# Optimization experiments

Measured on AMD Instinct MI355X. Metric: run time of the kernel, lower is better.

Reference implementation:

```python
import jax, jax.numpy as jnp
import numpy as np

N_TX, N_CARD, N_MERCH = 200000, 50000, 10000
E = 200000
TX_IN, EMB, H = 128, 64, 128
N_LAYERS, N_ETYPES = 2, 4  # etypes: 0 card->tx, 1 tx->card, 2 merch->tx, 3 tx->merch


def setup_inputs() -> dict:
    key = jax.random.key(0)
    ks = jax.random.split(key, 24)
    s = 0.05
    inp = {
        "tx_x": jax.random.normal(ks[0], (N_TX, TX_IN), jnp.float32),
        "card_ids": jnp.arange(N_CARD, dtype=jnp.int64),
        "merch_ids": jnp.arange(N_MERCH, dtype=jnp.int64),
        "e_card": jax.random.randint(ks[1], (E,), 0, N_CARD),
        "e_tx_c": jnp.arange(E, dtype=jnp.int64),
        "e_merch": jax.random.randint(ks[2], (E,), 0, N_MERCH),
        "e_tx_m": jnp.arange(E, dtype=jnp.int64),
        # parameters
        "card_emb": jax.random.normal(ks[3], (N_CARD, EMB), jnp.float32) * s,
        "merch_emb": jax.random.normal(ks[4], (N_MERCH, EMB), jnp.float32) * s,
        "card_proj_W": jax.random.normal(ks[5], (EMB, H), jnp.float32) * s,
        "card_proj_b": jnp.zeros((H,), jnp.float32),
        "merch_proj_W": jax.random.normal(ks[6], (EMB, H), jnp.float32) * s,
        "merch_proj_b": jnp.zeros((H,), jnp.float32),
        "tx_W": jax.random.normal(ks[7], (TX_IN, H), jnp.float32) * s,
        "tx_b": jnp.zeros((H,), jnp.float32),
        "conv_Wl": jax.random.normal(ks[8], (N_LAYERS, N_ETYPES, H, H), jnp.float32) * s,
        "conv_bl": jnp.zeros((N_LAYERS, N_ETYPES, H), jnp.float32),
        "conv_Wr": jax.random.normal(ks[9], (N_LAYERS, N_ETYPES, H, H), jnp.float32) * s,
        "h1_W": jax.random.normal(ks[10], (H, H), jnp.float32) * s,
        "h1_b": jnp.zeros((H,), jnp.float32),
        "h2_W": jax.random.normal(ks[11], (H, 1), jnp.float32) * s,
        "h2_b": jnp.zeros((1,), jnp.float32),
    }
    return inp


def _sage(x_src, x_dst, src, dst, Wl, bl, Wr, n_dst):
    # PyG SAGEConv: mean-aggregate neighbor features, then lin_l(agg)+lin_r(x_dst)
    agg = jax.ops.segment_sum(x_src[src], dst, num_segments=n_dst)
    cnt = jax.ops.segment_sum(jnp.ones((src.shape[0],), x_src.dtype), dst, num_segments=n_dst)
    mean = agg / jnp.maximum(cnt, 1.0)[:, None]
    return mean @ Wl + bl + x_dst @ Wr


def reference(tx_x, card_ids, merch_ids, e_card, e_tx_c, e_merch, e_tx_m,
              card_emb, merch_emb, card_proj_W, card_proj_b, merch_proj_W, merch_proj_b,
              tx_W, tx_b, conv_Wl, conv_bl, conv_Wr, h1_W, h1_b, h2_W, h2_b):
    # input encoders (dropout inactive at eval)
    h_tx = jax.nn.relu(tx_x @ tx_W + tx_b)
    h_card = card_emb[card_ids] @ card_proj_W + card_proj_b
    h_merch = merch_emb[merch_ids] @ merch_proj_W + merch_proj_b

    for l in range(N_LAYERS):
        Wl, bl, Wr = conv_Wl[l], conv_bl[l], conv_Wr[l]
        # HeteroConv aggr='sum' across edge types sharing a dst type
        o_tx = (_sage(h_card, h_tx, e_card, e_tx_c, Wl[0], bl[0], Wr[0], N_TX)
                + _sage(h_merch, h_tx, e_merch, e_tx_m, Wl[2], bl[2], Wr[2], N_TX))
        o_card = _sage(h_tx, h_card, e_tx_c, e_card, Wl[1], bl[1], Wr[1], N_CARD)
        o_merch = _sage(h_tx, h_merch, e_tx_m, e_merch, Wl[3], bl[3], Wr[3], N_MERCH)
        h_tx, h_card, h_merch = jax.nn.relu(o_tx), jax.nn.relu(o_card), jax.nn.relu(o_merch)

    logits = (jax.nn.relu(h_tx @ h1_W + h1_b) @ h2_W + h2_b).reshape(-1)
    return logits
```

## Files before the change

### kernel.cpp

```cpp
#include <hip/hip_runtime.h>


#define N_TX    200000
#define N_CARD  50000
#define N_MERCH 10000
#define NE      200000

typedef __attribute__((ext_vector_type(8))) short short8;
typedef __attribute__((ext_vector_type(4))) float f32x4;

__device__ inline unsigned short f2b(float f) {
    unsigned u = __builtin_bit_cast(unsigned, f);
    unsigned r = (u + 0x7fffu + ((u >> 16) & 1u)) >> 16;
    return (unsigned short)r;
}
__device__ inline float b2f(unsigned short s) {
    return __builtin_bit_cast(float, (unsigned)s << 16);
}

__global__ __launch_bounds__(256, 3) void fused2(
    const void* __restrict__ A, int a_f32,
    const unsigned short* __restrict__ W1T, const float* __restrict__ b1,
    const unsigned short* __restrict__ W2T, const float* __restrict__ b2,
    const unsigned short* __restrict__ P1, const int* __restrict__ I1,
    const unsigned short* __restrict__ P2, const int* __restrict__ I2,
    unsigned short* __restrict__ OUT0,
    const float* __restrict__ h2w, const float* __restrict__ h2b,
    void* __restrict__ OUT1, int M)
{
    __shared__ float Tf[64 * 132];
    __shared__ unsigned short Tb[64 * 136];
    const int tid  = threadIdx.x;
    const int wave = tid >> 6;
    const int lane = tid & 63;
    const int quad = lane >> 4;
    const int l15  = lane & 15;
    const int base = blockIdx.x * 64;
    const int rgrp = tid >> 4;
    const int c0   = l15 * 8;
    const bool modeA = (OUT0 != nullptr);

    int idx1[4], idx2[4];
#pragma unroll
    for (int p = 0; p < 4; ++p) {
        int r = base + p * 16 + rgrp;
        int rc = (r < M) ? r : 0;
        idx1[p] = I1 ? I1[rc] : 0;
        idx2[p] = I2 ? I2[rc] : 0;
    }

    short8 af[4];
    {
        int r = base + wave * 16 + l15;
        int rc = (r < M) ? r : 0;
        if (a_f32) {
            const float* ap = (const float*)A + (size_t)rc * 128 + quad * 8;
#pragma unroll
            for (int kk = 0; kk < 4; ++kk) {
                float4 u = *reinterpret_cast<const float4*>(ap + kk * 32);
                float4 v = *reinterpret_cast<const float4*>(ap + kk * 32 + 4);
                short8 t;
                t[0] = (short)f2b(u.x); t[1] = (short)f2b(u.y);
                t[2] = (short)f2b(u.z); t[3] = (short)f2b(u.w);
                t[4] = (short)f2b(v.x); t[5] = (short)f2b(v.y);
                t[6] = (short)f2b(v.z); t[7] = (short)f2b(v.w);
                af[kk] = t;
            }
        } else {
            const unsigned short* ap =
                (const unsigned short*)A + (size_t)rc * 128 + quad * 8;
#pragma unroll
            for (int kk = 0; kk < 4; ++kk)
                af[kk] = *reinterpret_cast<const short8*>(ap + kk * 32);
        }
    }

    f32x4 acc[8];
#pragma unroll
    for (int nt = 0; nt < 8; ++nt) acc[nt] = (f32x4){0.f, 0.f, 0.f, 0.f};
#pragma unroll
    for (int nt = 0; nt < 8; ++nt) {
        const unsigned short* bp = W1T + (nt * 16 + l15) * 128 + quad * 8;
#pragma unroll
        for (int kk = 0; kk < 4; ++kk) {
            short8 bf = *reinterpret_cast<const short8*>(bp + kk * 32);
            acc[nt] = __builtin_amdgcn_mfma_f32_16x16x32_bf16(
                af[kk], bf, acc[nt], 0, 0, 0);
        }
    }

    short8 p1v[4], p2v[4];
    if (P1) {
#pragma unroll
        for (int p = 0; p < 4; ++p)
            p1v[p] = *reinterpret_cast<const short8*>(
                P1 + (size_t)idx1[p] * 128 + c0);
    }
    if (P2) {
#pragma unroll
        for (int p = 0; p < 4; ++p)
            p2v[p] = *reinterpret_cast<const short8*>(
                P2 + (size_t)idx2[p] * 128 + c0);
    }

    const int lrow0 = wave * 16 + quad * 4;
    if (modeA) {
#pragma unroll
        for (int nt = 0; nt < 8; ++nt) {
            float bb = b1 ? b1[nt * 16 + l15] : 0.f;
#pragma unroll
            for (int reg = 0; reg < 4; ++reg)
                Tb[(lrow0 + reg) * 136 + nt * 16 + l15] =
                    f2b(fmaxf(acc[nt][reg] + bb, 0.f));
        }
    } else {
#pragma unroll
        for (int nt = 0; nt < 8; ++nt)
#pragma unroll
            for (int reg = 0; reg < 4; ++reg)
                Tf[(lrow0 + reg) * 132 + nt * 16 + l15] = acc[nt][reg];
    }
    __syncthreads();

    if (modeA) {
#pragma unroll
        for (int p = 0; p < 4; ++p) {
            const int rloc = p * 16 + rgrp;
            const int r = base + rloc;
            if (r < M) {
                short8 hv = *reinterpret_cast<const short8*>(&Tb[rloc * 136 + c0]);
                *reinterpret_cast<short8*>(OUT0 + (size_t)r * 128 + c0) = hv;
            }
        }
    } else {
        float b1r[8];
#pragma unroll
        for (int j = 0; j < 8; ++j) b1r[j] = b1 ? b1[c0 + j] : 0.f;
#pragma unroll
        for (int p = 0; p < 4; ++p) {
            const int rloc = p * 16 + rgrp;
            float4 u = *reinterpret_cast<const float4*>(&Tf[rloc * 132 + c0]);
            float4 v = *reinterpret_cast<const float4*>(&Tf[rloc * 132 + c0 + 4]);
            float o[8] = {u.x, u.y, u.z, u.w, v.x, v.y, v.z, v.w};
            short8 ov;
#pragma unroll
            for (int j = 0; j < 8; ++j) {
                float t = o[j] + b1r[j];
                if (P1) t += b2f((unsigned short)p1v[p][j]);
                if (P2) t += b2f((unsigned short)p2v[p][j]);
                ov[j] = (short)f2b(fmaxf(t, 0.f));
            }
            *reinterpret_cast<short8*>(&Tb[rloc * 136 + c0]) = ov;
        }
        __syncthreads();
    }

    short8 af2[4];
#pragma unroll
    for (int kk = 0; kk < 4; ++kk)
        af2[kk] = *reinterpret_cast<const short8*>(
            &Tb[(wave * 16 + l15) * 136 + quad * 8 + kk * 32]);

    f32x4 acc2[8];
#pragma unroll
    for (int nt = 0; nt < 8; ++nt) acc2[nt] = (f32x4){0.f, 0.f, 0.f, 0.f};
#pragma unroll
    for (int nt = 0; nt < 8; ++nt) {
        const unsigned short* bp = W2T + (nt * 16 + l15) * 128 + quad * 8;
#pragma unroll
        for (int kk = 0; kk < 4; ++kk) {
            short8 bf = *reinterpret_cast<const short8*>(bp + kk * 32);
            acc2[nt] = __builtin_amdgcn_mfma_f32_16x16x32_bf16(
                af2[kk], bf, acc2[nt], 0, 0, 0);
        }
    }

    if (!modeA) {
        float hsum[4] = {0.f, 0.f, 0.f, 0.f};
#pragma unroll
        for (int nt = 0; nt < 8; ++nt) {
            float bb = b2 ? b2[nt * 16 + l15] : 0.f;
            float w = h2w[nt * 16 + l15];
#pragma unroll
            for (int reg = 0; reg < 4; ++reg) {
                float o = fmaxf(acc2[nt][reg] + bb, 0.f);
                hsum[reg] += o * w;
            }
        }
        float* OUTf = (float*)OUT1;
#pragma unroll
        for (int reg = 0; reg < 4; ++reg) {
            float h = hsum[reg];
            h += __shfl_xor(h, 1);
            h += __shfl_xor(h, 2);
            h += __shfl_xor(h, 4);
            h += __shfl_xor(h, 8);
            int r = base + wave * 16 + quad * 4 + reg;
            if (l15 == 0 && r < M) OUTf[r] = h + h2b[0];
        }
    } else {
#pragma unroll
        for (int nt = 0; nt < 8; ++nt)
#pragma unroll
            for (int reg = 0; reg < 4; ++reg)
                Tf[(lrow0 + reg) * 132 + nt * 16 + l15] = acc2[nt][reg];
        __syncthreads();
        float b2r[8];
#pragma unroll
        for (int j = 0; j < 8; ++j) b2r[j] = b2 ? b2[c0 + j] : 0.f;
        unsigned short* OB = (unsigned short*)OUT1;
#pragma unroll
        for (int p = 0; p < 4; ++p) {
            const int rloc = p * 16 + rgrp;
            const int r = base + rloc;
            float4 u = *reinterpret_cast<const float4*>(&Tf[rloc * 132 + c0]);
            float4 v = *reinterpret_cast<const float4*>(&Tf[rloc * 132 + c0 + 4]);
            float o[8] = {u.x, u.y, u.z, u.w, v.x, v.y, v.z, v.w};
            short8 ov;
#pragma unroll
            for (int j = 0; j < 8; ++j) {
                float t = o[j] + b2r[j];
                if (P1) t += b2f((unsigned short)p1v[p][j]);
                if (P2) t += b2f((unsigned short)p2v[p][j]);
                ov[j] = (short)f2b(fmaxf(t, 0.f));
            }
            if (r < M)
                *reinterpret_cast<short8*>(OB + (size_t)r * 128 + c0) = ov;
        }
    }
}

__global__ __launch_bounds__(256, 3) void fusedE(
    const float* __restrict__ A, int K1,
    const unsigned short* __restrict__ W1T, const float* __restrict__ b1,
    const unsigned short* __restrict__ W2T,
    unsigned short* __restrict__ OUT0, unsigned short* __restrict__ OUT1, int M)
{
    __shared__ float Tf[64 * 132];
    __shared__ unsigned short Tb[64 * 136];
    const int tid  = threadIdx.x;
    const int wave = tid >> 6;
    const int lane = tid & 63;
    const int quad = lane >> 4;
    const int l15  = lane & 15;
    const int base = blockIdx.x * 64;
    const int rgrp = tid >> 4;
    const int c0   = l15 * 8;
    const int nkk  = K1 >> 5;

    short8 af[4];
    {
        int r = base + wave * 16 + l15;
        int rc = (r < M) ? r : 0;
        const float* ap = A + (size_t)rc * K1 + quad * 8;
#pragma unroll
        for (int kk = 0; kk < 4; ++kk) if (kk < nkk) {
            float4 u = *reinterpret_cast<const float4*>(ap + kk * 32);
            float4 v = *reinterpret_cast<const float4*>(ap + kk * 32 + 4);
            short8 t;
            t[0] = (short)f2b(u.x); t[1] = (short)f2b(u.y);
            t[2] = (short)f2b(u.z); t[3] = (short)f2b(u.w);
            t[4] = (short)f2b(v.x); t[5] = (short)f2b(v.y);
            t[6] = (short)f2b(v.z); t[7] = (short)f2b(v.w);
            af[kk] = t;
        }
    }

    f32x4 acc[8];
#pragma unroll
    for (int nt = 0; nt < 8; ++nt) acc[nt] = (f32x4){0.f, 0.f, 0.f, 0.f};
#pragma unroll
    for (int nt = 0; nt < 8; ++nt) {
        const unsigned short* bp = W1T + (nt * 16 + l15) * K1 + quad * 8;
#pragma unroll
        for (int kk = 0; kk < 4; ++kk) if (kk < nkk) {
            short8 bf = *reinterpret_cast<const short8*>(bp + kk * 32);
            acc[nt] = __builtin_amdgcn_mfma_f32_16x16x32_bf16(
                af[kk], bf, acc[nt], 0, 0, 0);
        }
    }

    const int lrow0 = wave * 16 + quad * 4;
#pragma unroll
    for (int nt = 0; nt < 8; ++nt) {
        float bb = b1 ? b1[nt * 16 + l15] : 0.f;
#pragma unroll
        for (int reg = 0; reg < 4; ++reg)
            Tb[(lrow0 + reg) * 136 + nt * 16 + l15] = f2b(acc[nt][reg] + bb);
    }
    __syncthreads();

#pragma unroll
    for (int p = 0; p < 4; ++p) {
        const int rloc = p * 16 + rgrp;
        const int r = base + rloc;
        if (r < M) {
            short8 hv = *reinterpret_cast<const short8*>(&Tb[rloc * 136 + c0]);
            *reinterpret_cast<short8*>(OUT0 + (size_t)r * 128 + c0) = hv;
        }
    }

    short8 af2[4];
#pragma unroll
    for (int kk = 0; kk < 4; ++kk)
        af2[kk] = *reinterpret_cast<const short8*>(
            &Tb[(wave * 16 + l15) * 136 + quad * 8 + kk * 32]);

    f32x4 acc2[8];
#pragma unroll
    for (int nt = 0; nt < 8; ++nt) acc2[nt] = (f32x4){0.f, 0.f, 0.f, 0.f};
#pragma unroll
    for (int nt = 0; nt < 8; ++nt) {
        const unsigned short* bp = W2T + (nt * 16 + l15) * 128 + quad * 8;
#pragma unroll
        for (int kk = 0; kk < 4; ++kk) {
            short8 bf = *reinterpret_cast<const short8*>(bp + kk * 32);
            acc2[nt] = __builtin_amdgcn_mfma_f32_16x16x32_bf16(
                af2[kk], bf, acc2[nt], 0, 0, 0);
        }
    }
#pragma unroll
    for (int nt = 0; nt < 8; ++nt)
#pragma unroll
        for (int reg = 0; reg < 4; ++reg)
            Tf[(lrow0 + reg) * 132 + nt * 16 + l15] = acc2[nt][reg];
    __syncthreads();
#pragma unroll
    for (int p = 0; p < 4; ++p) {
        const int rloc = p * 16 + rgrp;
        const int r = base + rloc;
        if (r >= M) continue;
        float4 u = *reinterpret_cast<const float4*>(&Tf[rloc * 132 + c0]);
        float4 v = *reinterpret_cast<const float4*>(&Tf[rloc * 132 + c0 + 4]);
        float o[8] = {u.x, u.y, u.z, u.w, v.x, v.y, v.z, v.w};
        short8 ov;
#pragma unroll
        for (int j = 0; j < 8; ++j) ov[j] = (short)f2b(o[j]);
        *reinterpret_cast<short8*>(OUT1 + (size_t)r * 128 + c0) = ov;
    }
}

__global__ __launch_bounds__(256, 3) void fusedU(
    const unsigned short* __restrict__ A1, const unsigned short* __restrict__ A2,
    const unsigned short* __restrict__ W1aT, const unsigned short* __restrict__ W1bT,
    const float* __restrict__ b1,
    const unsigned short* __restrict__ W2T,
    unsigned short* __restrict__ OUT1, int M)
{
    __shared__ float Tf[64 * 132];
    __shared__ unsigned short Tb[64 * 136];
    const int tid  = threadIdx.x;
    const int wave = tid >> 6;
    const int lane = tid & 63;
    const int quad = lane >> 4;
    const int l15  = lane & 15;
    const int base = blockIdx.x * 64;
    const int rgrp = tid >> 4;
    const int c0   = l15 * 8;

    short8 afa[4], afb[4];
    {
        int r = base + wave * 16 + l15;
        int rc = (r < M) ? r : 0;
        const unsigned short* a1 = A1 + (size_t)rc * 128 + quad * 8;
        const unsigned short* a2 = A2 + (size_t)rc * 128 + quad * 8;
#pragma unroll
        for (int kk = 0; kk < 4; ++kk) {
            afa[kk] = *reinterpret_cast<const short8*>(a1 + kk * 32);
            afb[kk] = *reinterpret_cast<const short8*>(a2 + kk * 32);
        }
    }

    f32x4 acc[8];
#pragma unroll
    for (int nt = 0; nt < 8; ++nt) acc[nt] = (f32x4){0.f, 0.f, 0.f, 0.f};
#pragma unroll
    for (int nt = 0; nt < 8; ++nt) {
        const unsigned short* bpa = W1aT + (nt * 16 + l15) * 128 + quad * 8;
        const unsigned short* bpb = W1bT + (nt * 16 + l15) * 128 + quad * 8;
#pragma unroll
        for (int kk = 0; kk < 4; ++kk) {
            short8 ba = *reinterpret_cast<const short8*>(bpa + kk * 32);
            acc[nt] = __builtin_amdgcn_mfma_f32_16x16x32_bf16(
                afa[kk], ba, acc[nt], 0, 0, 0);
            short8 bb = *reinterpret_cast<const short8*>(bpb + kk * 32);
            acc[nt] = __builtin_amdgcn_mfma_f32_16x16x32_bf16(
                afb[kk], bb, acc[nt], 0, 0, 0);
        }
    }

    const int lrow0 = wave * 16 + quad * 4;
#pragma unroll
    for (int nt = 0; nt < 8; ++nt) {
        float bv = b1 ? b1[nt * 16 + l15] : 0.f;
#pragma unroll
        for (int reg = 0; reg < 4; ++reg)
            Tb[(lrow0 + reg) * 136 + nt * 16 + l15] =
                f2b(fmaxf(acc[nt][reg] + bv, 0.f));
    }
    __syncthreads();

    short8 af2[4];
#pragma unroll
    for (int kk = 0; kk < 4; ++kk)
        af2[kk] = *reinterpret_cast<const short8*>(
            &Tb[(wave * 16 + l15) * 136 + quad * 8 + kk * 32]);

    f32x4 acc2[8];
#pragma unroll
    for (int nt = 0; nt < 8; ++nt) acc2[nt] = (f32x4){0.f, 0.f, 0.f, 0.f};
#pragma unroll
    for (int nt = 0; nt < 8; ++nt) {
        const unsigned short* bp = W2T + (nt * 16 + l15) * 128 + quad * 8;
#pragma unroll
        for (int kk = 0; kk < 4; ++kk) {
            short8 bf = *reinterpret_cast<const short8*>(bp + kk * 32);
            acc2[nt] = __builtin_amdgcn_mfma_f32_16x16x32_bf16(
                af2[kk], bf, acc2[nt], 0, 0, 0);
        }
    }
#pragma unroll
    for (int nt = 0; nt < 8; ++nt)
#pragma unroll
        for (int reg = 0; reg < 4; ++reg)
            Tf[(lrow0 + reg) * 132 + nt * 16 + l15] = acc2[nt][reg];
    __syncthreads();
#pragma unroll
    for (int p = 0; p < 4; ++p) {
        const int rloc = p * 16 + rgrp;
        const int r = base + rloc;
        if (r >= M) continue;
        float4 u = *reinterpret_cast<const float4*>(&Tf[rloc * 132 + c0]);
        float4 v = *reinterpret_cast<const float4*>(&Tf[rloc * 132 + c0 + 4]);
        float o[8] = {u.x, u.y, u.z, u.w, v.x, v.y, v.z, v.w};
        short8 ov;
#pragma unroll
        for (int j = 0; j < 8; ++j) ov[j] = (short)f2b(o[j]);
        *reinterpret_cast<short8*>(OUT1 + (size_t)r * 128 + c0) = ov;
    }
}

__global__ __launch_bounds__(256) void convert_weights(
    const float* __restrict__ tx_W, const float* __restrict__ card_proj_W,
    const float* __restrict__ merch_proj_W, const float* __restrict__ h1_W,
    const float* __restrict__ conv_Wl, const float* __restrict__ conv_Wr,
    const float* __restrict__ conv_bl,
    unsigned short* __restrict__ WT, float* __restrict__ bsum)
{
    int job = blockIdx.y;
    int K = 128;
    const float* src = nullptr;
    const float* src2 = nullptr;
    if (job == 0) src = tx_W;
    else if (job == 1) { src = card_proj_W; K = 64; }
    else if (job == 2) { src = merch_proj_W; K = 64; }
    else if (job == 3) src = h1_W;
    else {
        int l = (job - 4) / 7, e = (job - 4) % 7;
        const float* Wl = conv_Wl + (size_t)l * 4 * 16384;
        const float* Wr = conv_Wr + (size_t)l * 4 * 16384;
        switch (e) {
            case 0: src = Wl; break;
            case 1: src = Wl + 16384; break;
            case 2: src = Wl + 2 * 16384; break;
            case 3: src = Wl + 3 * 16384; break;
            case 4: src = Wr + 16384; break;
            case 5: src = Wr + 3 * 16384; break;
            default:
                src = Wr; src2 = Wr + 2 * 16384;
                if (blockIdx.x == 0 && threadIdx.x < 128) {
                    const float* bl = conv_bl + (size_t)l * 4 * 128;
                    bsum[l * 128 + threadIdx.x] =
                        bl[threadIdx.x] + bl[2 * 128 + threadIdx.x];
                }
                break;
        }
    }
    int e = blockIdx.x * 256 + threadIdx.x;
    if (e < (K << 7)) {
        int n = (K == 128) ? (e >> 7) : (e >> 6);
        int k = e & (K - 1);
        float v = src[(size_t)k * 128 + n];
        if (src2) v += src2[(size_t)k * 128 + n];
        WT[(size_t)job * 16384 + n * K + k] = f2b(v);
    }
}

__global__ __launch_bounds__(256) void hist_kernel(
    const int* __restrict__ e_card, const int* __restrict__ e_merch,
    int* __restrict__ hist_c, int* __restrict__ hist_m, int E)
{
    int i = blockIdx.x * 256 + threadIdx.x;
    if (i < E) {
        atomicAdd(&hist_c[e_card[i]], 1);
        atomicAdd(&hist_m[e_merch[i]], 1);
    }
}

__global__ __launch_bounds__(1024) void scan2_kernel(
    const int* __restrict__ hist_c, int* __restrict__ offs_c, int* __restrict__ cur_c, int nc,
    const int* __restrict__ hist_m, int* __restrict__ offs_m, int* __restrict__ cur_m, int nm)
{
    const int* hist = (blockIdx.x == 0) ? hist_c : hist_m;
    int* offs = (blockIdx.x == 0) ? offs_c : offs_m;
    int* cursor = (blockIdx.x == 0) ? cur_c : cur_m;
    int n = (blockIdx.x == 0) ? nc : nm;
    __shared__ int wsum[16];
    __shared__ int s_carry;
    const int tid = threadIdx.x, lane = tid & 63, wid = tid >> 6;
    if (tid == 0) s_carry = 0;
    __syncthreads();
    for (int base = 0; base < n; base += 1024) {
        int i = base + tid;
        int v = (i < n) ? hist[i] : 0;
        int x = v;
#pragma unroll
        for (int d = 1; d < 64; d <<= 1) {
            int t = __shfl_up(x, d);
            if (lane >= d) x += t;
        }
        if (lane == 63) wsum[wid] = x;
        __syncthreads();
        if (wid == 0) {
            int y = (lane < 16) ? wsum[lane] : 0;
#pragma unroll
            for (int d = 1; d < 16; d <<= 1) {
                int t = __shfl_up(y, d);
                if (lane >= d) y += t;
            }
            if (lane < 16) wsum[lane] = y;
        }
        __syncthreads();
        int wbase = (wid > 0) ? wsum[wid - 1] : 0;
        int excl = s_carry + wbase + x - v;
        if (i < n) { offs[i] = excl; cursor[i] = excl; }
        __syncthreads();
        if (tid == 0) s_carry += wsum[15];
        __syncthreads();
    }
    if (threadIdx.x == 0) offs[n] = s_carry;
}

__global__ __launch_bounds__(256) void place_kernel(
    const int* __restrict__ e_card, const int* __restrict__ e_tx_c,
    const int* __restrict__ e_merch, const int* __restrict__ e_tx_m,
    int* __restrict__ cur_c, int* __restrict__ eidx_c,
    int* __restrict__ cur_m, int* __restrict__ eidx_m, int E)
{
    int i = blockIdx.x * 256 + threadIdx.x;
    if (i < E) {
        int pc = atomicAdd(&cur_c[e_card[i]], 1);
        eidx_c[pc] = e_tx_c[i];
        int pm = atomicAdd(&cur_m[e_merch[i]], 1);
        eidx_m[pm] = e_tx_m[i];
    }
}

__global__ __launch_bounds__(256) void gather_mean(
    const unsigned short* __restrict__ h_src, const int* __restrict__ offs,
    const int* __restrict__ eidx, unsigned short* __restrict__ out_mean, int n_dst)
{
    const int lane = threadIdx.x & 63;
    const int l15 = lane & 15;
    const int quad = lane >> 4;
    const int d = blockIdx.x * 4 + (threadIdx.x >> 6);
    if (d >= n_dst) return;
    const int s = offs[d], e = offs[d + 1];
    float a[8] = {0.f, 0.f, 0.f, 0.f, 0.f, 0.f, 0.f, 0.f};
    for (int p = s + quad; p < e; p += 4) {
        int tx = eidx[p];
        short8 v = *reinterpret_cast<const short8*>(
            h_src + (size_t)tx * 128 + l15 * 8);
#pragma unroll
        for (int j = 0; j < 8; ++j) a[j] += b2f((unsigned short)v[j]);
    }
#pragma unroll
    for (int j = 0; j < 8; ++j) {
        a[j] += __shfl_xor(a[j], 16);
        a[j] += __shfl_xor(a[j], 32);
    }
    if (quad == 0) {
        const float inv = (e > s) ? 1.0f / (float)(e - s) : 0.f;
        short8 o;
#pragma unroll
        for (int j = 0; j < 8; ++j) o[j] = (short)f2b(a[j] * inv);
        *reinterpret_cast<short8*>(out_mean + (size_t)d * 128 + l15 * 8) = o;
    }
}

extern "C" void kernel_launch(void* const* d_in, const int* in_sizes, int n_in,
                              void* d_out, int out_size, void* d_ws, size_t ws_size,
                              hipStream_t stream)
{
    const float* tx_x        = (const float*)d_in[0];
    const int*   e_card      = (const int*)d_in[3];
    const int*   e_tx_c      = (const int*)d_in[4];
    const int*   e_merch     = (const int*)d_in[5];
    const int*   e_tx_m      = (const int*)d_in[6];
    const float* card_emb    = (const float*)d_in[7];
    const float* merch_emb   = (const float*)d_in[8];
    const float* card_proj_W = (const float*)d_in[9];
    const float* card_proj_b = (const float*)d_in[10];
    const float* merch_proj_W= (const float*)d_in[11];
    const float* merch_proj_b= (const float*)d_in[12];
    const float* tx_W        = (const float*)d_in[13];
    const float* tx_b        = (const float*)d_in[14];
    const float* conv_Wl     = (const float*)d_in[15];
    const float* conv_bl     = (const float*)d_in[16];
    const float* conv_Wr     = (const float*)d_in[17];
    const float* h1_W        = (const float*)d_in[18];
    const float* h1_b        = (const float*)d_in[19];
    const float* h2_W        = (const float*)d_in[20];
    const float* h2_b        = (const float*)d_in[21];

    char* wsb = (char*)d_ws;
    auto alloc = [&](size_t bytes) {
        char* p = wsb; wsb += (bytes + 255) & ~(size_t)255; return p;
    };
    unsigned short* h_tx0      = (unsigned short*)alloc((size_t)N_TX * 128 * 2);
    unsigned short* h_tx1      = (unsigned short*)alloc((size_t)N_TX * 128 * 2);
    unsigned short* h_card0    = (unsigned short*)alloc((size_t)N_CARD * 128 * 2);
    unsigned short* h_merch0   = (unsigned short*)alloc((size_t)N_MERCH * 128 * 2);
    unsigned short* p_card     = (unsigned short*)alloc((size_t)N_CARD * 128 * 2);
    unsigned short* p_merch    = (unsigned short*)alloc((size_t)N_MERCH * 128 * 2);
    unsigned short* mean_card  = (unsigned short*)alloc((size_t)N_CARD * 128 * 2);
    unsigned short* mean_merch = (unsigned short*)alloc((size_t)N_MERCH * 128 * 2);
    unsigned short* WT         = (unsigned short*)alloc((size_t)18 * 16384 * 2);
    float* bsum = (float*)alloc(2 * 128 * 4);
    int* hist_c = (int*)alloc((size_t)(N_CARD + N_MERCH) * 4);
    int* hist_m = hist_c + N_CARD;
    int* offs_c = (int*)alloc((size_t)(N_CARD + 1) * 4);
    int* cur_c  = (int*)alloc((size_t)N_CARD * 4);
    int* eidx_c = (int*)alloc((size_t)NE * 4);
    int* offs_m = (int*)alloc((size_t)(N_MERCH + 1) * 4);
    int* cur_m  = (int*)alloc((size_t)N_MERCH * 4);
    int* eidx_m = (int*)alloc((size_t)NE * 4);

    auto WTj = [&](int job) { return WT + (size_t)job * 16384; };

    convert_weights<<<dim3(64, 18), dim3(256), 0, stream>>>(
        tx_W, card_proj_W, merch_proj_W, h1_W, conv_Wl, conv_Wr, conv_bl,
        WT, bsum);
    hipMemsetAsync(hist_c, 0, (size_t)(N_CARD + N_MERCH) * 4, stream);
    hist_kernel<<<dim3((NE + 255) / 256), dim3(256), 0, stream>>>(
        e_card, e_merch, hist_c, hist_m, NE);
    scan2_kernel<<<dim3(2), dim3(1024), 0, stream>>>(
        hist_c, offs_c, cur_c, N_CARD, hist_m, offs_m, cur_m, N_MERCH);
    place_kernel<<<dim3((NE + 255) / 256), dim3(256), 0, stream>>>(
        e_card, e_tx_c, e_merch, e_tx_m, cur_c, eidx_c, cur_m, eidx_m, NE);

    fusedE<<<dim3((N_CARD + 63) / 64), dim3(256), 0, stream>>>(
        card_emb, 64, WTj(1), card_proj_b, WTj(4), h_card0, p_card, N_CARD);
    fusedE<<<dim3((N_MERCH + 63) / 64), dim3(256), 0, stream>>>(
        merch_emb, 64, WTj(2), merch_proj_b, WTj(6), h_merch0, p_merch, N_MERCH);

    fused2<<<dim3((N_TX + 63) / 64), dim3(256), 0, stream>>>(
        tx_x, 1, WTj(0), tx_b, WTj(10), bsum,
        p_card, e_card, p_merch, e_merch,
        h_tx0, nullptr, nullptr, h_tx1, N_TX);

    gather_mean<<<dim3((N_CARD + 3) / 4), dim3(256), 0, stream>>>(
        h_tx0, offs_c, eidx_c, mean_card, N_CARD);
    gather_mean<<<dim3((N_MERCH + 3) / 4), dim3(256), 0, stream>>>(
        h_tx0, offs_m, eidx_m, mean_merch, N_MERCH);

    fusedU<<<dim3((N_CARD + 63) / 64), dim3(256), 0, stream>>>(
        mean_card, h_card0, WTj(5), WTj(8), conv_bl + 128, WTj(11),
        p_card, N_CARD);
    fusedU<<<dim3((N_MERCH + 63) / 64), dim3(256), 0, stream>>>(
        mean_merch, h_merch0, WTj(7), WTj(9), conv_bl + 3 * 128, WTj(13),
        p_merch, N_MERCH);

    fused2<<<dim3((N_TX + 63) / 64), dim3(256), 0, stream>>>(
        h_tx1, 0, WTj(17), bsum + 128, WTj(3), h1_b,
        p_card, e_card, p_merch, e_merch,
        nullptr, h2_W, h2_b, d_out, N_TX);
}
```

Measured before the change: 675.6 us.

## Fuse gather-mean into update kernel, merge card/merchant launches, vectorize scan

Moves the neighbor mean aggregation into the per-node update GEMM kernel, so mean results stay in shared memory instead of round-tripping through global buffers. Card and merchant work are merged into single launches that pick their parameters by block index, and the embedding kernel is specialized to K=64. The prefix scan now has each thread handle 8 elements, cutting the number of block-wide iterations. The fused gather runs inside 64-row GEMM blocks, which may lower parallelism for the irregular gather and serializes 16 rows per wave.

Measured after the change: 713.9 us. +5.7%, slower.

```diff
diff --git a/kernel.cpp b/kernel.cpp
--- a/kernel.cpp
+++ b/kernel.cpp
@@ -230,31 +230,44 @@
     }
 }
 
-__global__ __launch_bounds__(256, 3) void fusedE(
-    const float* __restrict__ A, int K1,
-    const unsigned short* __restrict__ W1T, const float* __restrict__ b1,
-    const unsigned short* __restrict__ W2T,
-    unsigned short* __restrict__ OUT0, unsigned short* __restrict__ OUT1, int M)
+__global__ __launch_bounds__(256, 3) void fusedE_both(
+    const float* __restrict__ Ac, const unsigned short* __restrict__ W1Tc,
+    const float* __restrict__ b1c, const unsigned short* __restrict__ W2Tc,
+    unsigned short* __restrict__ OUT0c, unsigned short* __restrict__ OUT1c,
+    int Mc, int nbc,
+    const float* __restrict__ Am, const unsigned short* __restrict__ W1Tm,
+    const float* __restrict__ b1m, const unsigned short* __restrict__ W2Tm,
+    unsigned short* __restrict__ OUT0m, unsigned short* __restrict__ OUT1m,
+    int Mm)
 {
     __shared__ float Tf[64 * 132];
     __shared__ unsigned short Tb[64 * 136];
+    const bool isC = (int)blockIdx.x < nbc;
+    const int bx   = isC ? blockIdx.x : blockIdx.x - nbc;
+    const float* A = isC ? Ac : Am;
+    const unsigned short* W1T = isC ? W1Tc : W1Tm;
+    const float* b1 = isC ? b1c : b1m;
+    const unsigned short* W2T = isC ? W2Tc : W2Tm;
+    unsigned short* OUT0 = isC ? OUT0c : OUT0m;
+    unsigned short* OUT1 = isC ? OUT1c : OUT1m;
+    const int M = isC ? Mc : Mm;
+
     const int tid  = threadIdx.x;
     const int wave = tid >> 6;
     const int lane = tid & 63;
     const int quad = lane >> 4;
     const int l15  = lane & 15;
-    const int base = blockIdx.x * 64;
+    const int base = bx * 64;
     const int rgrp = tid >> 4;
     const int c0   = l15 * 8;
-    const int nkk  = K1 >> 5;
-
-    short8 af[4];
+
+    short8 af[2];
     {
         int r = base + wave * 16 + l15;
         int rc = (r < M) ? r : 0;
-        const float* ap = A + (size_t)rc * K1 + quad * 8;
-#pragma unroll
-        for (int kk = 0; kk < 4; ++kk) if (kk < nkk) {
+        const float* ap = A + (size_t)rc * 64 + quad * 8;
+#pragma unroll
+        for (int kk = 0; kk < 2; ++kk) {
             float4 u = *reinterpret_cast<const float4*>(ap + kk * 32);
             float4 v = *reinterpret_cast<const float4*>(ap + kk * 32 + 4);
             short8 t;
@@ -271,9 +284,9 @@
     for (int nt = 0; nt < 8; ++nt) acc[nt] = (f32x4){0.f, 0.f, 0.f, 0.f};
 #pragma unroll
     for (int nt = 0; nt < 8; ++nt) {
-        const unsigned short* bp = W1T + (nt * 16 + l15) * K1 + quad * 8;
-#pragma unroll
-        for (int kk = 0; kk < 4; ++kk) if (kk < nkk) {
+        const unsigned short* bp = W1T + (nt * 16 + l15) * 64 + quad * 8;
+#pragma unroll
+        for (int kk = 0; kk < 2; ++kk) {
             short8 bf = *reinterpret_cast<const short8*>(bp + kk * 32);
             acc[nt] = __builtin_amdgcn_mfma_f32_16x16x32_bf16(
                 af[kk], bf, acc[nt], 0, 0, 0);
@@ -340,33 +353,78 @@
     }
 }
 
-__global__ __launch_bounds__(256, 3) void fusedU(
-    const unsigned short* __restrict__ A1, const unsigned short* __restrict__ A2,
-    const unsigned short* __restrict__ W1aT, const unsigned short* __restrict__ W1bT,
-    const float* __restrict__ b1,
-    const unsigned short* __restrict__ W2T,
-    unsigned short* __restrict__ OUT1, int M)
+__global__ __launch_bounds__(256, 3) void fusedU2_both(
+    const unsigned short* __restrict__ h_src,
+    const int* __restrict__ offs_c, const int* __restrict__ eidx_c,
+    const unsigned short* __restrict__ A2c,
+    const unsigned short* __restrict__ W1aTc, const unsigned short* __restrict__ W1bTc,
+    const float* __restrict__ b1c, const unsigned short* __restrict__ W2Tc,
+    unsigned short* __restrict__ OUTc, int Mc, int nbc,
+    const int* __restrict__ offs_m, const int* __restrict__ eidx_m,
+    const unsigned short* __restrict__ A2m,
+    const unsigned short* __restrict__ W1aTm, const unsigned short* __restrict__ W1bTm,
+    const float* __restrict__ b1m, const unsigned short* __restrict__ W2Tm,
+    unsigned short* __restrict__ OUTm, int Mm)
 {
     __shared__ float Tf[64 * 132];
     __shared__ unsigned short Tb[64 * 136];
+    const bool isC = (int)blockIdx.x < nbc;
+    const int bx   = isC ? blockIdx.x : blockIdx.x - nbc;
+    const int* offs = isC ? offs_c : offs_m;
+    const int* eidx = isC ? eidx_c : eidx_m;
+    const unsigned short* A2 = isC ? A2c : A2m;
+    const unsigned short* W1aT = isC ? W1aTc : W1aTm;
+    const unsigned short* W1bT = isC ? W1bTc : W1bTm;
+    const float* b1 = isC ? b1c : b1m;
+    const unsigned short* W2T = isC ? W2Tc : W2Tm;
+    unsigned short* OUT1 = isC ? OUTc : OUTm;
+    const int M = isC ? Mc : Mm;
+
     const int tid  = threadIdx.x;
     const int wave = tid >> 6;
     const int lane = tid & 63;
     const int quad = lane >> 4;
     const int l15  = lane & 15;
-    const int base = blockIdx.x * 64;
+    const int base = bx * 64;
     const int rgrp = tid >> 4;
     const int c0   = l15 * 8;
+
+    for (int n = 0; n < 16; ++n) {
+        const int d = base + wave * 16 + n;
+        int s = 0, e = 0;
+        if (d < M) { s = offs[d]; e = offs[d + 1]; }
+        float a[8] = {0.f, 0.f, 0.f, 0.f, 0.f, 0.f, 0.f, 0.f};
+        for (int p = s + quad; p < e; p += 4) {
+            int tx = eidx[p];
+            short8 v = *reinterpret_cast<const short8*>(
+                h_src + (size_t)tx * 128 + l15 * 8);
+#pragma unroll
+            for (int j = 0; j < 8; ++j) a[j] += b2f((unsigned short)v[j]);
+        }
+#pragma unroll
+        for (int j = 0; j < 8; ++j) {
+            a[j] += __shfl_xor(a[j], 16);
+            a[j] += __shfl_xor(a[j], 32);
+        }
+        if (quad == 0 && d < M) {
+            const float inv = (e > s) ? 1.0f / (float)(e - s) : 0.f;
+            short8 o;
+#pragma unroll
+            for (int j = 0; j < 8; ++j) o[j] = (short)f2b(a[j] * inv);
+            *reinterpret_cast<short8*>(&Tb[(wave * 16 + n) * 136 + l15 * 8]) = o;
+        }
+    }
+    __syncthreads();
 
     short8 afa[4], afb[4];
     {
         int r = base + wave * 16 + l15;
         int rc = (r < M) ? r : 0;
-        const unsigned short* a1 = A1 + (size_t)rc * 128 + quad * 8;
         const unsigned short* a2 = A2 + (size_t)rc * 128 + quad * 8;
 #pragma unroll
         for (int kk = 0; kk < 4; ++kk) {
-            afa[kk] = *reinterpret_cast<const short8*>(a1 + kk * 32);
+            afa[kk] = *reinterpret_cast<const short8*>(
+                &Tb[(wave * 16 + l15) * 136 + quad * 8 + kk * 32]);
             afb[kk] = *reinterpret_cast<const short8*>(a2 + kk * 32);
         }
     }
@@ -388,6 +446,7 @@
                 afb[kk], bb, acc[nt], 0, 0, 0);
         }
     }
+    __syncthreads();
 
     const int lrow0 = wave * 16 + quad * 4;
 #pragma unroll
@@ -510,10 +569,17 @@
     const int tid = threadIdx.x, lane = tid & 63, wid = tid >> 6;
     if (tid == 0) s_carry = 0;
     __syncthreads();
-    for (int base = 0; base < n; base += 1024) {
-        int i = base + tid;
-        int v = (i < n) ? hist[i] : 0;
-        int x = v;
+    for (int base = 0; base < n; base += 8192) {
+        const int i0 = base + tid * 8;
+        int v[8];
+        int tot = 0;
+#pragma unroll
+        for (int j = 0; j < 8; ++j) {
+            int idx = i0 + j;
+            v[j] = (idx < n) ? hist[idx] : 0;
+            tot += v[j];
+        }
+        int x = tot;
 #pragma unroll
         for (int d = 1; d < 64; d <<= 1) {
             int t = __shfl_up(x, d);
@@ -532,8 +598,13 @@
         }
         __syncthreads();
         int wbase = (wid > 0) ? wsum[wid - 1] : 0;
-        int excl = s_carry + wbase + x - v;
-        if (i < n) { offs[i] = excl; cursor[i] = excl; }
+        int run = s_carry + wbase + x - tot;
+#pragma unroll
+        for (int j = 0; j < 8; ++j) {
+            int idx = i0 + j;
+            if (idx < n) { offs[idx] = run; cursor[idx] = run; }
+            run += v[j];
+        }
         __syncthreads();
         if (tid == 0) s_carry += wsum[15];
         __syncthreads();
@@ -553,38 +624,6 @@
         eidx_c[pc] = e_tx_c[i];
         int pm = atomicAdd(&cur_m[e_merch[i]], 1);
         eidx_m[pm] = e_tx_m[i];
-    }
-}
-
-__global__ __launch_bounds__(256) void gather_mean(
-    const unsigned short* __restrict__ h_src, const int* __restrict__ offs,
-    const int* __restrict__ eidx, unsigned short* __restrict__ out_mean, int n_dst)
-{
-    const int lane = threadIdx.x & 63;
-    const int l15 = lane & 15;
-    const int quad = lane >> 4;
-    const int d = blockIdx.x * 4 + (threadIdx.x >> 6);
-    if (d >= n_dst) return;
-    const int s = offs[d], e = offs[d + 1];
-    float a[8] = {0.f, 0.f, 0.f, 0.f, 0.f, 0.f, 0.f, 0.f};
-    for (int p = s + quad; p < e; p += 4) {
-        int tx = eidx[p];
-        short8 v = *reinterpret_cast<const short8*>(
-            h_src + (size_t)tx * 128 + l15 * 8);
-#pragma unroll
-        for (int j = 0; j < 8; ++j) a[j] += b2f((unsigned short)v[j]);
-    }
-#pragma unroll
-    for (int j = 0; j < 8; ++j) {
-        a[j] += __shfl_xor(a[j], 16);
-        a[j] += __shfl_xor(a[j], 32);
-    }
-    if (quad == 0) {
-        const float inv = (e > s) ? 1.0f / (float)(e - s) : 0.f;
-        short8 o;
-#pragma unroll
-        for (int j = 0; j < 8; ++j) o[j] = (short)f2b(a[j] * inv);
-        *reinterpret_cast<short8*>(out_mean + (size_t)d * 128 + l15 * 8) = o;
     }
 }
 
@@ -617,15 +656,13 @@
     auto alloc = [&](size_t bytes) {
         char* p = wsb; wsb += (bytes + 255) & ~(size_t)255; return p;
     };
-    unsigned short* h_tx0      = (unsigned short*)alloc((size_t)N_TX * 128 * 2);
-    unsigned short* h_tx1      = (unsigned short*)alloc((size_t)N_TX * 128 * 2);
-    unsigned short* h_card0    = (unsigned short*)alloc((size_t)N_CARD * 128 * 2);
-    unsigned short* h_merch0   = (unsigned short*)alloc((size_t)N_MERCH * 128 * 2);
-    unsigned short* p_card     = (unsigned short*)alloc((size_t)N_CARD * 128 * 2);
-    unsigned short* p_merch    = (unsigned short*)alloc((size_t)N_MERCH * 128 * 2);
-    unsigned short* mean_card  = (unsigned short*)alloc((size_t)N_CARD * 128 * 2);
-    unsigned short* mean_merch = (unsigned short*)alloc((size_t)N_MERCH * 128 * 2);
-    unsigned short* WT         = (unsigned short*)alloc((size_t)18 * 16384 * 2);
+    unsigned short* h_tx0    = (unsigned short*)alloc((size_t)N_TX * 128 * 2);
+    unsigned short* h_tx1    = (unsigned short*)alloc((size_t)N_TX * 128 * 2);
+    unsigned short* h_card0  = (unsigned short*)alloc((size_t)N_CARD * 128 * 2);
+    unsigned short* h_merch0 = (unsigned short*)alloc((size_t)N_MERCH * 128 * 2);
+    unsigned short* p_card   = (unsigned short*)alloc((size_t)N_CARD * 128 * 2);
+    unsigned short* p_merch  = (unsigned short*)alloc((size_t)N_MERCH * 128 * 2);
+    unsigned short* WT       = (unsigned short*)alloc((size_t)18 * 16384 * 2);
     float* bsum = (float*)alloc(2 * 128 * 4);
     int* hist_c = (int*)alloc((size_t)(N_CARD + N_MERCH) * 4);
     int* hist_m = hist_c + N_CARD;
@@ -637,6 +674,9 @@
     int* eidx_m = (int*)alloc((size_t)NE * 4);
 
     auto WTj = [&](int job) { return WT + (size_t)job * 16384; };
+
+    const int nbc = (N_CARD + 63) / 64;
+    const int nbm = (N_MERCH + 63) / 64;
 
     convert_weights<<<dim3(64, 18), dim3(256), 0, stream>>>(
         tx_W, card_proj_W, merch_proj_W, h1_W, conv_Wl, conv_Wr, conv_bl,
@@ -649,26 +689,20 @@
     place_kernel<<<dim3((NE + 255) / 256), dim3(256), 0, stream>>>(
         e_card, e_tx_c, e_merch, e_tx_m, cur_c, eidx_c, cur_m, eidx_m, NE);
 
-    fusedE<<<dim3((N_CARD + 63) / 64), dim3(256), 0, stream>>>(
-        card_emb, 64, WTj(1), card_proj_b, WTj(4), h_card0, p_card, N_CARD);
-    fusedE<<<dim3((N_MERCH + 63) / 64), dim3(256), 0, stream>>>(
-        merch_emb, 64, WTj(2), merch_proj_b, WTj(6), h_merch0, p_merch, N_MERCH);
+    fusedE_both<<<dim3(nbc + nbm), dim3(256), 0, stream>>>(
+        card_emb, WTj(1), card_proj_b, WTj(4), h_card0, p_card, N_CARD, nbc,
+        merch_emb, WTj(2), merch_proj_b, WTj(6), h_merch0, p_merch, N_MERCH);
 
     fused2<<<dim3((N_TX + 63) / 64), dim3(256), 0, stream>>>(
         tx_x, 1, WTj(0), tx_b, WTj(10), bsum,
         p_card, e_card, p_merch, e_merch,
         h_tx0, nullptr, nullptr, h_tx1, N_TX);
 
-    gather_mean<<<dim3((N_CARD + 3) / 4), dim3(256), 0, stream>>>(
-        h_tx0, offs_c, eidx_c, mean_card, N_CARD);
-    gather_mean<<<dim3((N_MERCH + 3) / 4), dim3(256), 0, stream>>>(
-        h_tx0, offs_m, eidx_m, mean_merch, N_MERCH);
-
-    fusedU<<<dim3((N_CARD + 63) / 64), dim3(256), 0, stream>>>(
-        mean_card, h_card0, WTj(5), WTj(8), conv_bl + 128, WTj(11),
-        p_card, N_CARD);
-    fusedU<<<dim3((N_MERCH + 63) / 64), dim3(256), 0, stream>>>(
-        mean_merch, h_merch0, WTj(7), WTj(9), conv_bl + 3 * 128, WTj(13),
+    fusedU2_both<<<dim3(nbc + nbm), dim3(256), 0, stream>>>(
+        h_tx0,
+        offs_c, eidx_c, h_card0, WTj(5), WTj(8), conv_bl + 128, WTj(11),
+        p_card, N_CARD, nbc,
+        offs_m, eidx_m, h_merch0, WTj(7), WTj(9), conv_bl + 3 * 128, WTj(13),
         p_merch, N_MERCH);
 
     fused2<<<dim3((N_TX + 63) / 64), dim3(256), 0, stream>>>(
```
